# Performance work log

Measured on AMD Instinct MI355X. Metric: run time of the kernel, lower is better.

Reference implementation:

```python
import jax, jax.numpy as jnp
import numpy as np

SPLIT = 3  # split_num: number of lead groups

def _hw_flatten(t, split):
    # [B,H,W,C] -> split along H into `split` groups, concat groups on channel axis,
    # then flatten spatial dims: result [B, (H/split)*W, split*C]
    B, H, W, C = t.shape
    hs = H // split
    t = t.reshape(B, split, hs, W, C).transpose(0, 2, 3, 1, 4)  # [B,hs,W,split,C]
    return t.reshape(B, hs * W, split * C)

def _hw_recover(o, B, hs, W, split, C):
    # inverse of _hw_flatten: [B, hs*W, split*C] -> [B, split*hs, W, C]
    o = o.reshape(B, hs, W, split, C).transpose(0, 3, 1, 2, 4)
    return o.reshape(B, split * hs, W, C)

def setup_inputs() -> dict:
    key = jax.random.key(0)
    kx, kf, kg, kh, kgam = jax.random.split(key, 5)
    B, H, W, C = 32, 12, 256, 256
    scale = 8
    Cf = C // scale
    x = jax.random.normal(kx, (B, H, W, C), dtype=jnp.float32)
    # 1x1 conv kernels == channel-mixing matrices [C_in, C_out], glorot-ish scale
    Wf = jax.random.normal(kf, (C, Cf), dtype=jnp.float32) * (2.0 / (C + Cf)) ** 0.5
    Wg = jax.random.normal(kg, (C, Cf), dtype=jnp.float32) * (2.0 / (C + Cf)) ** 0.5
    Wh = jax.random.normal(kh, (C, C), dtype=jnp.float32) * (1.0 / C) ** 0.5
    gamma = jax.random.normal(kgam, (1,), dtype=jnp.float32) * 0.1
    return {"x": x, "Wf": Wf, "Wg": Wg, "Wh": Wh, "gamma": gamma}

def reference(x, Wf, Wg, Wh, gamma):
    B, H, W, C = x.shape
    hs = H // SPLIT
    # 1x1 convs are per-pixel channel matmuls
    f = jnp.einsum('bhwc,cd->bhwd', x, Wf)
    g = jnp.einsum('bhwc,cd->bhwd', x, Wg)
    h = jnp.einsum('bhwc,cd->bhwd', x, Wh)
    f_fl = _hw_flatten(f, SPLIT)  # [B, N, SPLIT*Cf]
    g_fl = _hw_flatten(g, SPLIT)  # [B, N, SPLIT*Cf]
    h_fl = _hw_flatten(h, SPLIT)  # [B, N, SPLIT*C]
    # s = g @ f^T : [B, N, N]
    s = jnp.einsum('bnc,bmc->bnm', g_fl, f_fl)
    beta = jax.nn.softmax(s, axis=-1)
    o = jnp.einsum('bnm,bmc->bnc', beta, h_fl)  # [B, N, SPLIT*C]
    o = _hw_recover(o, B, hs, W, SPLIT, C)      # [B, H, W, C]
    return gamma * o + x
```

## Files before the change

### kernel.cpp

```cpp
#include <hip/hip_runtime.h>


typedef __bf16 bf16x8 __attribute__((ext_vector_type(8)));
typedef float f32x4 __attribute__((ext_vector_type(4)));

#define MFMA16 __builtin_amdgcn_mfma_f32_16x16x32_bf16

__device__ __forceinline__ short f2bf(float f) {
    unsigned u = __builtin_bit_cast(unsigned, f);
    u += 0x7fffu + ((u >> 16) & 1u);
    return (short)(u >> 16);
}
__device__ __forceinline__ unsigned pack2bf(float a, float b) {
    return ((unsigned)(unsigned short)f2bf(a)) |
           (((unsigned)(unsigned short)f2bf(b)) << 16);
}
__device__ __forceinline__ unsigned encf(float f) {
    unsigned u = __builtin_bit_cast(unsigned, f);
    return ((int)u < 0) ? ~u : (u | 0x80000000u);
}
__device__ __forceinline__ float decf(unsigned u) {
    unsigned v = (u & 0x80000000u) ? (u & 0x7fffffffu) : ~u;
    return __builtin_bit_cast(float, v);
}
__device__ __forceinline__ void gload_lds16(const short* g, short* l) {
    __builtin_amdgcn_global_load_lds(
        (const __attribute__((address_space(1))) unsigned int*)g,
        (__attribute__((address_space(3))) unsigned int*)l, 16, 0, 0);
}

__global__ __launch_bounds__(256) void wt_kernel(const float* __restrict__ Wf,
                                                 const float* __restrict__ Wg,
                                                 const float* __restrict__ Wh,
                                                 short* __restrict__ Wt) {
    int t = blockIdx.x * 256 + threadIdx.x;
    int j = t >> 8, k = t & 255;
    float v;
    if (j < 32)      v = Wf[k * 32 + j];
    else if (j < 64) v = Wg[k * 32 + (j - 32)];
    else             v = Wh[k * 256 + (j - 64)];
    Wt[j * 256 + k] = f2bf(v);
}

__global__ __launch_bounds__(256) void proj_kernel(const float* __restrict__ x,
                                                   const short* __restrict__ Wt,
                                                   short* __restrict__ f_fl,
                                                   short* __restrict__ g_fl,
                                                   short* __restrict__ h_t) {
    const int tid = threadIdx.x;
    const int P0  = blockIdx.x * 64;
    const int b   = P0 / 3072;
    const int rem = P0 % 3072;
    const int hh  = rem >> 8;
    const int wbase = rem & 255;
    const int lead = hh >> 2, hsi = hh & 3;
    const int nbase = hsi * 256 + wbase;

    __shared__ __align__(16) short xs[64][264];

    const float4* xv = (const float4*)(x + (size_t)P0 * 256);
    #pragma unroll
    for (int i = 0; i < 16; ++i) {
        int idx = i * 256 + tid;
        float4 v = xv[idx];
        int pix = idx >> 6;
        int col = (idx & 63) * 4;
        *(short4*)&xs[pix][col] =
            make_short4(f2bf(v.x), f2bf(v.y), f2bf(v.z), f2bf(v.w));
    }
    __syncthreads();

    const int lane = tid & 63, wv = tid >> 6;
    const int quad = lane >> 4, l15 = lane & 15;

    {
        const int jrow = wv * 16 + l15;
        f32x4 acc[4] = {};
        #pragma unroll
        for (int ki = 0; ki < 8; ++ki) {
            bf16x8 a = *(const bf16x8*)&Wt[jrow * 256 + ki * 32 + quad * 8];
            #pragma unroll
            for (int pt = 0; pt < 4; ++pt) {
                bf16x8 bb = *(const bf16x8*)&xs[pt * 16 + l15][ki * 32 + quad * 8];
                acc[pt] = MFMA16(a, bb, acc[pt], 0, 0, 0);
            }
        }
        short* dst = (wv < 2) ? f_fl : g_fl;
        const int jloc = (wv & 1) * 16 + quad * 4;
        #pragma unroll
        for (int pt = 0; pt < 4; ++pt) {
            int n = nbase + pt * 16 + l15;
            *(short4*)&dst[((size_t)b * 1024 + n) * 96 + lead * 32 + jloc] =
                make_short4(f2bf(acc[pt][0]), f2bf(acc[pt][1]),
                            f2bf(acc[pt][2]), f2bf(acc[pt][3]));
        }
    }

    {
        f32x4 acc[4][4] = {};
        #pragma unroll
        for (int ki = 0; ki < 8; ++ki) {
            bf16x8 a[4], bb[4];
            #pragma unroll
            for (int pt = 0; pt < 4; ++pt)
                a[pt] = *(const bf16x8*)&xs[pt * 16 + l15][ki * 32 + quad * 8];
            #pragma unroll
            for (int ct = 0; ct < 4; ++ct)
                bb[ct] = *(const bf16x8*)&Wt[(64 + wv * 64 + ct * 16 + l15) * 256 + ki * 32 + quad * 8];
            #pragma unroll
            for (int pt = 0; pt < 4; ++pt)
                #pragma unroll
                for (int ct = 0; ct < 4; ++ct)
                    acc[pt][ct] = MFMA16(a[pt], bb[ct], acc[pt][ct], 0, 0, 0);
        }
        #pragma unroll
        for (int pt = 0; pt < 4; ++pt)
            #pragma unroll
            for (int ct = 0; ct < 4; ++ct) {
                int cc = wv * 64 + ct * 16 + l15;
                size_t base = ((size_t)b * 768 + lead * 256 + cc) * 1024
                              + nbase + pt * 16 + quad * 4;
                *(short4*)&h_t[base] =
                    make_short4(f2bf(acc[pt][ct][0]), f2bf(acc[pt][ct][1]),
                                f2bf(acc[pt][ct][2]), f2bf(acc[pt][ct][3]));
            }
    }
}

__global__ __launch_bounds__(256) void smax_kernel(const short* __restrict__ f_fl,
                                                   const short* __restrict__ g_fl,
                                                   unsigned* __restrict__ menc) {
    const int kt = blockIdx.x, qt = blockIdx.y, b = blockIdx.z;
    const int tid = threadIdx.x, lane = tid & 63, wv = tid >> 6;
    const int quad = lane >> 4, l15 = lane & 15;
    const int wm = (wv & 1) * 64, wn = (wv >> 1) * 64;
    const short* fB = f_fl + ((size_t)b * 1024 + kt * 128 + wm) * 96;
    const short* gB = g_fl + ((size_t)b * 1024 + qt * 128 + wn) * 96;

    bf16x8 bfr[4][3];
    #pragma unroll
    for (int j = 0; j < 4; ++j)
        #pragma unroll
        for (int ki = 0; ki < 3; ++ki)
            bfr[j][ki] = *(const bf16x8*)&gB[(j * 16 + l15) * 96 + ki * 32 + quad * 8];

    f32x4 acc[4][4] = {};
    #pragma unroll
    for (int i = 0; i < 4; ++i) {
        bf16x8 a[3];
        #pragma unroll
        for (int ki = 0; ki < 3; ++ki)
            a[ki] = *(const bf16x8*)&fB[(i * 16 + l15) * 96 + ki * 32 + quad * 8];
        #pragma unroll
        for (int j = 0; j < 4; ++j)
            #pragma unroll
            for (int ki = 0; ki < 3; ++ki)
                acc[i][j] = MFMA16(a[ki], bfr[j][ki], acc[i][j], 0, 0, 0);
    }

    #pragma unroll
    for (int j = 0; j < 4; ++j) {
        float v = acc[0][j][0];
        #pragma unroll
        for (int i = 0; i < 4; ++i)
            #pragma unroll
            for (int r = 0; r < 4; ++r) v = fmaxf(v, acc[i][j][r]);
        v = fmaxf(v, __shfl_xor(v, 16));
        v = fmaxf(v, __shfl_xor(v, 32));
        if (quad == 0)
            atomicMax(&menc[b * 1024 + qt * 128 + wn + j * 16 + l15], encf(v));
    }
}

__global__ __launch_bounds__(256) void pexp_kernel(const short* __restrict__ f_fl,
                                                   const short* __restrict__ g_fl,
                                                   const unsigned* __restrict__ menc,
                                                   float* __restrict__ lsum,
                                                   short* __restrict__ P) {
    const int kt = blockIdx.x, qt = blockIdx.y, b = blockIdx.z;
    const int tid = threadIdx.x, lane = tid & 63, wv = tid >> 6;
    const int quad = lane >> 4, l15 = lane & 15;
    const int wm = (wv & 1) * 64, wn = (wv >> 1) * 64;
    const short* fB = f_fl + ((size_t)b * 1024 + kt * 128 + wm) * 96;
    const short* gB = g_fl + ((size_t)b * 1024 + qt * 128 + wn) * 96;

    bf16x8 bfr[4][3];
    #pragma unroll
    for (int j = 0; j < 4; ++j)
        #pragma unroll
        for (int ki = 0; ki < 3; ++ki)
            bfr[j][ki] = *(const bf16x8*)&gB[(j * 16 + l15) * 96 + ki * 32 + quad * 8];

    f32x4 acc[4][4] = {};
    #pragma unroll
    for (int i = 0; i < 4; ++i) {
        bf16x8 a[3];
        #pragma unroll
        for (int ki = 0; ki < 3; ++ki)
            a[ki] = *(const bf16x8*)&fB[(i * 16 + l15) * 96 + ki * 32 + quad * 8];
        #pragma unroll
        for (int j = 0; j < 4; ++j)
            #pragma unroll
            for (int ki = 0; ki < 3; ++ki)
                acc[i][j] = MFMA16(a[ki], bfr[j][ki], acc[i][j], 0, 0, 0);
    }

    short* Pb = (short*)P + (size_t)b * 1024 * 1024;
    #pragma unroll
    for (int j = 0; j < 4; ++j) {
        const int qrow = qt * 128 + wn + j * 16 + l15;
        const float mj = decf(menc[b * 1024 + qrow]);
        float rs = 0.f;
        #pragma unroll
        for (int i = 0; i < 4; ++i) {
            float e0 = __expf(acc[i][j][0] - mj);
            float e1 = __expf(acc[i][j][1] - mj);
            float e2 = __expf(acc[i][j][2] - mj);
            float e3 = __expf(acc[i][j][3] - mj);
            rs += (e0 + e1) + (e2 + e3);
            uint2 w;
            w.x = pack2bf(e0, e1);
            w.y = pack2bf(e2, e3);
            *(uint2*)&Pb[(size_t)qrow * 1024 + kt * 128 + wm + i * 16 + quad * 4] = w;
        }
        rs += __shfl_xor(rs, 16);
        rs += __shfl_xor(rs, 32);
        if (quad == 0)
            atomicAdd(&lsum[b * 1024 + qrow], rs);
    }
}

__global__ __launch_bounds__(256, 2) void gemm_kernel(const short* __restrict__ P,
                                                      const short* __restrict__ h_t,
                                                      const float* __restrict__ lsum,
                                                      const float* __restrict__ x,
                                                      const float* __restrict__ gammap,
                                                      float* __restrict__ out) {
    const int wgid = blockIdx.x;
    const int xcd  = wgid & 7;
    const int slot = wgid >> 3;
    const int b    = xcd * 4 + (slot / 48);
    const int t    = slot % 48;
    const int mt   = t % 6;
    const int nt   = t / 6;

    const int tid = threadIdx.x, lane = tid & 63, wv = tid >> 6;
    const int quad = lane >> 4, l15 = lane & 15;
    const int wm = (wv & 1) * 64, wn = (wv >> 1) * 64;

    __shared__ __align__(16) short As[2][128 * 32];
    __shared__ __align__(16) short Bs[2][128 * 32];

    const short* hB = h_t + ((size_t)b * 768 + mt * 128) * 1024;
    const short* Pb = P + ((size_t)b * 1024 + nt * 128) * 1024;

    const int srow  = wv * 16 + (lane >> 2);
    const int chunk = lane & 3;
    const int csw   = chunk ^ ((lane >> 3) & 3);
    const short* gA0 = hB + (size_t)srow * 1024 + csw * 8;
    const short* gA1 = hB + (size_t)(srow + 64) * 1024 + csw * 8;
    const short* gB0 = Pb + (size_t)srow * 1024 + csw * 8;
    const short* gB1 = Pb + (size_t)(srow + 64) * 1024 + csw * 8;
    const int ldst = srow * 32 + chunk * 8;

    const int ca = (quad ^ ((l15 >> 1) & 3)) * 8;

    f32x4 acc[4][4] = {};

    gload_lds16(gA0, &As[0][ldst]);
    gload_lds16(gA1, &As[0][ldst + 64 * 32]);
    gload_lds16(gB0, &Bs[0][ldst]);
    gload_lds16(gB1, &Bs[0][ldst + 64 * 32]);
    __syncthreads();

    int cur = 0;
    for (int kt = 0; kt < 32; ++kt) {
        if (kt < 31) {
            const int k0 = (kt + 1) * 32;
            short* a0 = &As[cur ^ 1][ldst];
            short* b0 = &Bs[cur ^ 1][ldst];
            gload_lds16(gA0 + k0, a0);
            gload_lds16(gA1 + k0, a0 + 64 * 32);
            gload_lds16(gB0 + k0, b0);
            gload_lds16(gB1 + k0, b0 + 64 * 32);
        }
        bf16x8 a[4], bb[4];
        #pragma unroll
        for (int i = 0; i < 4; ++i)
            a[i] = *(const bf16x8*)&As[cur][(wm + i * 16 + l15) * 32 + ca];
        #pragma unroll
        for (int j = 0; j < 4; ++j)
            bb[j] = *(const bf16x8*)&Bs[cur][(wn + j * 16 + l15) * 32 + ca];
        #pragma unroll
        for (int i = 0; i < 4; ++i)
            #pragma unroll
            for (int j = 0; j < 4; ++j)
                acc[i][j] = MFMA16(a[i], bb[j], acc[i][j], 0, 0, 0);
        __syncthreads();
        cur ^= 1;
    }

    const float gamma = gammap[0];
    float gl[4];
    #pragma unroll
    for (int j = 0; j < 4; ++j)
        gl[j] = gamma / lsum[b * 1024 + nt * 128 + wn + j * 16 + l15];

    #pragma unroll
    for (int i = 0; i < 4; ++i)
        #pragma unroll
        for (int j = 0; j < 4; ++j) {
            int vc = mt * 128 + wm + i * 16 + quad * 4;
            int qrow = nt * 128 + wn + j * 16 + l15;
            int lead = vc >> 8, c = vc & 255;
            int hsi = qrow >> 8, w_ = qrow & 255;
            size_t idx = (((size_t)b * 12 + lead * 4 + hsi) * 256 + w_) * 256 + c;
            float4 xv = *(const float4*)&x[idx];
            float4 ov;
            ov.x = gl[j] * acc[i][j][0] + xv.x;
            ov.y = gl[j] * acc[i][j][1] + xv.y;
            ov.z = gl[j] * acc[i][j][2] + xv.z;
            ov.w = gl[j] * acc[i][j][3] + xv.w;
            *(float4*)&out[idx] = ov;
        }
}

extern "C" void kernel_launch(void* const* d_in, const int* in_sizes, int n_in,
                              void* d_out, int out_size, void* d_ws, size_t ws_size,
                              hipStream_t stream) {
    const float* x     = (const float*)d_in[0];
    const float* Wf    = (const float*)d_in[1];
    const float* Wg    = (const float*)d_in[2];
    const float* Wh    = (const float*)d_in[3];
    const float* gamma = (const float*)d_in[4];
    float* out = (float*)d_out;

    char* ws = (char*)d_ws;
    short*    Wt   = (short*)(ws + 0);
    short*    f_fl = (short*)(ws + 163840);
    short*    g_fl = (short*)(ws + 6455296);
    short*    h_t  = (short*)(ws + 12746752);
    short*    P    = (short*)(ws + 63078400);
    unsigned* menc = (unsigned*)(ws + 130187264);
    float*    lsum = (float*)(ws + 130318336);

    hipMemsetAsync(menc, 0, 32 * 1024 * 4, stream);
    hipMemsetAsync(lsum, 0, 32 * 1024 * 4, stream);
    wt_kernel<<<dim3(320), dim3(256), 0, stream>>>(Wf, Wg, Wh, Wt);
    proj_kernel<<<dim3(1536), dim3(256), 0, stream>>>(x, Wt, f_fl, g_fl, h_t);
    smax_kernel<<<dim3(8, 8, 32), dim3(256), 0, stream>>>(f_fl, g_fl, menc);
    pexp_kernel<<<dim3(8, 8, 32), dim3(256), 0, stream>>>(f_fl, g_fl, menc, lsum, P);
    gemm_kernel<<<dim3(1536), dim3(256), 0, stream>>>(P, h_t, lsum, x, gamma, out);
}
```

Measured before the change: 379.0 us.

## Triple-buffer gemm LDS pipeline and fold memsets into weight kernel

The final GEMM moves from a double-buffered to a triple-buffered LDS pipeline. Tiles are prefetched two k-steps ahead, and the full __syncthreads is replaced by an explicit vmcnt wait plus s_barrier, so global-to-LDS loads overlap more with MFMA work. Launch bounds rise to three blocks per CU. The two hipMemsetAsync calls are removed and the zeroing of menc and lsum is done inside wt_kernel, saving two launches. The risks are higher LDS usage and register pressure at three blocks per CU, and correctness of the hand-tuned vmcnt counts.

Result: faster. 354.9 us (-6.4%).

```diff
diff --git a/kernel.cpp b/kernel.cpp
--- a/kernel.cpp
+++ b/kernel.cpp
@@ -32,8 +32,14 @@
 __global__ __launch_bounds__(256) void wt_kernel(const float* __restrict__ Wf,
                                                  const float* __restrict__ Wg,
                                                  const float* __restrict__ Wh,
-                                                 short* __restrict__ Wt) {
+                                                 short* __restrict__ Wt,
+                                                 unsigned* __restrict__ menc,
+                                                 float* __restrict__ lsum) {
     int t = blockIdx.x * 256 + threadIdx.x;
+    if (t < 32768) {
+        menc[t] = 0u;
+        lsum[t] = 0.f;
+    }
     int j = t >> 8, k = t & 255;
     float v;
     if (j < 32)      v = Wf[k * 32 + j];
@@ -230,7 +236,7 @@
     }
 }
 
-__global__ __launch_bounds__(256, 2) void gemm_kernel(const short* __restrict__ P,
+__global__ __launch_bounds__(256, 3) void gemm_kernel(const short* __restrict__ P,
                                                       const short* __restrict__ h_t,
                                                       const float* __restrict__ lsum,
                                                       const float* __restrict__ x,
@@ -248,8 +254,8 @@
     const int quad = lane >> 4, l15 = lane & 15;
     const int wm = (wv & 1) * 64, wn = (wv >> 1) * 64;
 
-    __shared__ __align__(16) short As[2][128 * 32];
-    __shared__ __align__(16) short Bs[2][128 * 32];
+    __shared__ __align__(16) short As[3][128 * 32];
+    __shared__ __align__(16) short Bs[3][128 * 32];
 
     const short* hB = h_t + ((size_t)b * 768 + mt * 128) * 1024;
     const short* Pb = P + ((size_t)b * 1024 + nt * 128) * 1024;
@@ -267,23 +273,29 @@
 
     f32x4 acc[4][4] = {};
 
-    gload_lds16(gA0, &As[0][ldst]);
-    gload_lds16(gA1, &As[0][ldst + 64 * 32]);
-    gload_lds16(gB0, &Bs[0][ldst]);
-    gload_lds16(gB1, &Bs[0][ldst + 64 * 32]);
-    __syncthreads();
+#define STAGE_TILE(ktile, bufidx) do {                        \
+        const int k0_ = (ktile) * 32;                         \
+        short* a0_ = &As[bufidx][ldst];                       \
+        short* b0_ = &Bs[bufidx][ldst];                       \
+        gload_lds16(gA0 + k0_, a0_);                          \
+        gload_lds16(gA1 + k0_, a0_ + 64 * 32);                \
+        gload_lds16(gB0 + k0_, b0_);                          \
+        gload_lds16(gB1 + k0_, b0_ + 64 * 32);                \
+    } while (0)
+
+    STAGE_TILE(0, 0);
+    STAGE_TILE(1, 1);
 
     int cur = 0;
     for (int kt = 0; kt < 32; ++kt) {
         if (kt < 31) {
-            const int k0 = (kt + 1) * 32;
-            short* a0 = &As[cur ^ 1][ldst];
-            short* b0 = &Bs[cur ^ 1][ldst];
-            gload_lds16(gA0 + k0, a0);
-            gload_lds16(gA1 + k0, a0 + 64 * 32);
-            gload_lds16(gB0 + k0, b0);
-            gload_lds16(gB1 + k0, b0 + 64 * 32);
-        }
+            asm volatile("s_waitcnt vmcnt(4)" ::: "memory");
+        } else {
+            asm volatile("s_waitcnt vmcnt(0)" ::: "memory");
+        }
+        __builtin_amdgcn_s_barrier();
+        __builtin_amdgcn_sched_barrier(0);
+
         bf16x8 a[4], bb[4];
         #pragma unroll
         for (int i = 0; i < 4; ++i)
@@ -291,14 +303,21 @@
         #pragma unroll
         for (int j = 0; j < 4; ++j)
             bb[j] = *(const bf16x8*)&Bs[cur][(wn + j * 16 + l15) * 32 + ca];
+
+        if (kt < 30) {
+            const int nx = (cur == 0) ? 2 : cur - 1;
+            STAGE_TILE(kt + 2, nx);
+        }
+
         #pragma unroll
         for (int i = 0; i < 4; ++i)
             #pragma unroll
             for (int j = 0; j < 4; ++j)
                 acc[i][j] = MFMA16(a[i], bb[j], acc[i][j], 0, 0, 0);
-        __syncthreads();
-        cur ^= 1;
-    }
+
+        cur = (cur == 2) ? 0 : cur + 1;
+    }
+#undef STAGE_TILE
 
     const float gamma = gammap[0];
     float gl[4];
@@ -344,9 +363,7 @@
     unsigned* menc = (unsigned*)(ws + 130187264);
     float*    lsum = (float*)(ws + 130318336);
 
-    hipMemsetAsync(menc, 0, 32 * 1024 * 4, stream);
-    hipMemsetAsync(lsum, 0, 32 * 1024 * 4, stream);
-    wt_kernel<<<dim3(320), dim3(256), 0, stream>>>(Wf, Wg, Wh, Wt);
+    wt_kernel<<<dim3(320), dim3(256), 0, stream>>>(Wf, Wg, Wh, Wt, menc, lsum);
     proj_kernel<<<dim3(1536), dim3(256), 0, stream>>>(x, Wt, f_fl, g_fl, h_t);
     smax_kernel<<<dim3(8, 8, 32), dim3(256), 0, stream>>>(f_fl, g_fl, menc);
     pexp_kernel<<<dim3(8, 8, 32), dim3(256), 0, stream>>>(f_fl, g_fl, menc, lsum, P);
```
